# Kernel tuning notes

Measured on AMD Instinct MI355X. Metric: run time of the kernel, lower is better.

The kernel has to match this reference:

```python
import jax, jax.numpy as jnp
import numpy as np

OUT_F, IN_F, GROUP = 4096, 4096, 64  # meta['shape'] = (OUT_F, IN_F), group_size=64, axis=1
TOKENS = 8192  # batch*seq flattened


def dequant(W_q, scale, zero):
    # unpack_4bit_u8: high nibble = first half of rows, low nibble = second half
    hi = (W_q >> 4).astype(jnp.float32)
    lo = (W_q & 0xF).astype(jnp.float32)
    W_r = jnp.concatenate([hi, lo], axis=0)      # [G, GROUP]
    W_r = (W_r - zero) * scale                   # group-wise dequant (axis=1 grouping)
    return W_r.reshape(OUT_F, IN_F)


def setup_inputs() -> dict:
    key = jax.random.key(0)
    k0, k1, k2, k3, k4 = jax.random.split(key, 5)
    G = OUT_F * IN_F // GROUP  # 262144 groups
    x = jax.random.normal(k0, (TOKENS, IN_F), dtype=jnp.float32)
    W_q = jax.random.randint(k1, (G // 2, GROUP), 0, 256, dtype=jnp.int32)  # packed bytes
    scale = jax.random.uniform(k2, (G, 1), dtype=jnp.float32) * 0.01 + 1e-4  # 1/scale from quantizer
    zero = jax.random.uniform(k3, (G, 1), dtype=jnp.float32) * 15.0
    bias = jax.random.normal(k4, (OUT_F,), dtype=jnp.float32)
    return {"x": x, "W_q": W_q, "scale": scale, "zero": zero, "bias": bias}


def reference(x, W_q, scale, zero, bias):
    # HQQMatmulNoCacheDeq.forward: out = x @ dequantize().T + bias
    W_r = dequant(W_q, scale, zero)              # [OUT_F, IN_F]
    return x @ W_r.T + bias                      # [TOKENS, OUT_F]
```

## Files before the change

kernel.cpp:

```cpp
#include <hip/hip_runtime.h>
#include <stdint.h>


typedef __attribute__((ext_vector_type(8))) _Float16 half8;
typedef __attribute__((ext_vector_type(4))) float f32x4;

#define M_DIM 8192
#define N_DIM 4096
#define K_DIM 4096

__device__ __forceinline__ void async16(const void* g, void* l) {
  __builtin_amdgcn_global_load_lds(
      (const __attribute__((address_space(1))) void*)g,
      (__attribute__((address_space(3))) void*)l,
      16, 0, 0);
}

__global__ __launch_bounds__(256) void prep(
    const float* __restrict__ x, const int* __restrict__ Wq,
    const float* __restrict__ scale, const float* __restrict__ zero,
    _Float16* __restrict__ xh, _Float16* __restrict__ wh) {
  const int b = blockIdx.x;
  if (b < 16384) {
    const size_t i = ((size_t)b * 256 + threadIdx.x) * 8;
    f32x4 a = *(const f32x4*)(x + i);
    f32x4 c = *(const f32x4*)(x + i + 4);
    half8 h;
    h[0] = (_Float16)a[0]; h[1] = (_Float16)a[1];
    h[2] = (_Float16)a[2]; h[3] = (_Float16)a[3];
    h[4] = (_Float16)c[0]; h[5] = (_Float16)c[1];
    h[6] = (_Float16)c[2]; h[7] = (_Float16)c[3];
    *(half8*)(xh + i) = h;
  } else {
    const int idx = (b - 16384) * 256 + threadIdx.x;
    const int o  = idx >> 9;
    const int kb = (idx & 511) << 3;
    const int g  = (o << 6) + (kb >> 6);
    const int j  = kb & 63;
    const bool hi = (o < 2048);
    const int* src = Wq + (size_t)(hi ? g : g - 131072) * 64 + j;
    const int4 v0 = *(const int4*)src;
    const int4 v1 = *(const int4*)(src + 4);
    const float s  = scale[g];
    const float nz = -zero[g] * s;
    int raw[8] = {v0.x, v0.y, v0.z, v0.w, v1.x, v1.y, v1.z, v1.w};
    half8 h;
#pragma unroll
    for (int r = 0; r < 8; ++r) {
      const int nib = hi ? ((raw[r] >> 4) & 0xF) : (raw[r] & 0xF);
      h[r] = (_Float16)((float)nib * s + nz);
    }
    *(half8*)(wh + (size_t)o * K_DIM + kb) = h;
  }
}

__global__ __launch_bounds__(512, 2) void gemm_f16_fine(
    const _Float16* __restrict__ A, const _Float16* __restrict__ B,
    const float* __restrict__ bias, float* __restrict__ C) {
  __shared__ _Float16 As[3 * 8192];
  __shared__ _Float16 Bs[3 * 8192];

  const int tid  = threadIdx.x;
  const int wave = tid >> 6;
  const int lane = tid & 63;
  const int quad = lane >> 4;
  const int l16  = lane & 15;
  const int wm   = wave >> 2;
  const int wn   = wave & 3;

  const int bid = blockIdx.x;
  const int swb = (bid & 7) * 64 + (bid >> 3);
  const int m0 = (swb >> 4) * 256;
  const int n0 = (swb & 15) * 256;

  const int srow = tid >> 2;
  const int sg   = (((tid & 3) ^ ((tid >> 3) & 3)) << 3);
  const _Float16* gA0 = A + (size_t)(m0 + srow) * K_DIM + sg;
  const _Float16* gA1 = gA0 + (size_t)128 * K_DIM;
  const _Float16* gB0 = B + (size_t)(n0 + srow) * K_DIM + sg;
  const _Float16* gB1 = gB0 + (size_t)128 * K_DIM;
  const int wst = wave * 512;

  const int fro  = ((quad ^ ((l16 >> 1) & 3)) << 3);
  const int arow = wm * 128 + l16;
  const int brow = wn * 64 + l16;

  f32x4 acc[8][4] = {};

  const int NT = K_DIM / 32;

  async16(gA0,      As + wst);
  async16(gA1,      As + 4096 + wst);
  async16(gB0,      Bs + wst);
  async16(gB1,      Bs + 4096 + wst);
  async16(gA0 + 32, As + 8192 + wst);
  async16(gA1 + 32, As + 8192 + 4096 + wst);
  async16(gB0 + 32, Bs + 8192 + wst);
  async16(gB1 + 32, Bs + 8192 + 4096 + wst);
  asm volatile("s_waitcnt vmcnt(4)" ::: "memory");
  __builtin_amdgcn_s_barrier();

#define KSTEP(SR, SW, T)                                                     \
  {                                                                          \
    half8 aF[4], bF[4];                                                      \
          \
    aF[0] = *(const half8*)(As + (SR) + (arow + 0 * 16) * 32 + fro);         \
    bF[0] = *(const half8*)(Bs + (SR) + (brow + 0 * 16) * 32 + fro);         \
    bF[1] = *(const half8*)(Bs + (SR) + (brow + 1 * 16) * 32 + fro);         \
    bF[2] = *(const half8*)(Bs + (SR) + (brow + 2 * 16) * 32 + fro);         \
    bF[3] = *(const half8*)(Bs + (SR) + (brow + 3 * 16) * 32 + fro);         \
    aF[1] = *(const half8*)(As + (SR) + (arow + 1 * 16) * 32 + fro);         \
    aF[2] = *(const half8*)(As + (SR) + (arow + 2 * 16) * 32 + fro);         \
    aF[3] = *(const half8*)(As + (SR) + (arow + 3 * 16) * 32 + fro);         \
    if ((T) + 2 < NT) {                                                      \
      const int kk = ((T) + 2) * 32;                                         \
      async16(gA0 + kk, As + (SW) + wst);                                    \
      async16(gA1 + kk, As + (SW) + 4096 + wst);                             \
    }                                                                        \
    __builtin_amdgcn_s_barrier();                                            \
    __builtin_amdgcn_s_setprio(1);                                           \
    _Pragma("unroll") for (int i = 0; i < 4; ++i)                            \
      _Pragma("unroll") for (int j = 0; j < 4; ++j)                          \
        acc[i][j] = __builtin_amdgcn_mfma_f32_16x16x32_f16(                  \
            aF[i], bF[j], acc[i][j], 0, 0, 0);                               \
    __builtin_amdgcn_s_setprio(0);                                           \
    __builtin_amdgcn_s_barrier();                                            \
          \
    aF[0] = *(const half8*)(As + (SR) + (arow + 64 + 0 * 16) * 32 + fro);    \
    aF[1] = *(const half8*)(As + (SR) + (arow + 64 + 1 * 16) * 32 + fro);    \
    aF[2] = *(const half8*)(As + (SR) + (arow + 64 + 2 * 16) * 32 + fro);    \
    aF[3] = *(const half8*)(As + (SR) + (arow + 64 + 3 * 16) * 32 + fro);    \
    if ((T) + 2 < NT) {                                                      \
      const int kk = ((T) + 2) * 32;                                         \
      async16(gB0 + kk, Bs + (SW) + wst);                                    \
      async16(gB1 + kk, Bs + (SW) + 4096 + wst);                             \
      asm volatile("s_waitcnt vmcnt(4)" ::: "memory");                       \
    } else {                                                                 \
      asm volatile("s_waitcnt vmcnt(0)" ::: "memory");                       \
    }                                                                        \
    __builtin_amdgcn_s_barrier();                                            \
    __builtin_amdgcn_s_setprio(1);                                           \
    _Pragma("unroll") for (int i = 0; i < 4; ++i)                            \
      _Pragma("unroll") for (int j = 0; j < 4; ++j)                          \
        acc[i + 4][j] = __builtin_amdgcn_mfma_f32_16x16x32_f16(              \
            aF[i], bF[j], acc[i + 4][j], 0, 0, 0);                           \
    __builtin_amdgcn_s_setprio(0);                                           \
    __builtin_amdgcn_s_barrier();                                            \
  }

  for (int T = 0; T < 126; T += 3) {
    KSTEP(0,     16384, T)
    KSTEP(8192,  0,     T + 1)
    KSTEP(16384, 8192,  T + 2)
  }
  KSTEP(0,    16384, 126)
  KSTEP(8192, 0,     127)
#undef KSTEP

#pragma unroll
  for (int j = 0; j < 4; ++j) {
    const int n = n0 + wn * 64 + j * 16 + l16;
    const float bv = bias[n];
#pragma unroll
    for (int i = 0; i < 8; ++i) {
      const int m = m0 + wm * 128 + i * 16 + quad * 4;
      float* p = C + (size_t)m * N_DIM + n;
      f32x4 v = acc[i][j];
      p[0 * N_DIM] = v[0] + bv;
      p[1 * N_DIM] = v[1] + bv;
      p[2 * N_DIM] = v[2] + bv;
      p[3 * N_DIM] = v[3] + bv;
    }
  }
}

__global__ __launch_bounds__(256) void gemm_fp32_fallback(
    const float* __restrict__ x, const int* __restrict__ Wq,
    const float* __restrict__ scale, const float* __restrict__ zero,
    const float* __restrict__ bias, float* __restrict__ C) {
  __shared__ float As[64][16];
  __shared__ float Bs[64][16];
  const int tid = threadIdx.x;
  const int m0 = blockIdx.y * 64;
  const int n0 = blockIdx.x * 64;
  const int tx = tid & 15;
  const int ty = tid >> 4;
  const int lr = tid >> 2;
  const int lc = (tid & 3) << 2;

  float acc[4][4] = {};

  for (int k0 = 0; k0 < K_DIM; k0 += 16) {
    __syncthreads();
    *(f32x4*)&As[lr][lc] = *(const f32x4*)(x + (size_t)(m0 + lr) * K_DIM + k0 + lc);
    {
      const int o = n0 + lr;
      const int k = k0 + lc;
      const int g = (o << 6) + (k >> 6);
      const bool hi = (o < 2048);
      const int* src = Wq + (size_t)(hi ? g : g - 131072) * 64 + (k & 63);
      const int4 v = *(const int4*)src;
      const float s = scale[g];
      const float nz = -zero[g] * s;
      f32x4 b;
      if (hi) {
        b[0] = (float)((v.x >> 4) & 0xF) * s + nz;
        b[1] = (float)((v.y >> 4) & 0xF) * s + nz;
        b[2] = (float)((v.z >> 4) & 0xF) * s + nz;
        b[3] = (float)((v.w >> 4) & 0xF) * s + nz;
      } else {
        b[0] = (float)(v.x & 0xF) * s + nz;
        b[1] = (float)(v.y & 0xF) * s + nz;
        b[2] = (float)(v.z & 0xF) * s + nz;
        b[3] = (float)(v.w & 0xF) * s + nz;
      }
      *(f32x4*)&Bs[lr][lc] = b;
    }
    __syncthreads();
#pragma unroll
    for (int kk = 0; kk < 16; ++kk) {
      float a[4], b[4];
#pragma unroll
      for (int r = 0; r < 4; ++r) a[r] = As[ty * 4 + r][kk];
#pragma unroll
      for (int c = 0; c < 4; ++c) b[c] = Bs[tx * 4 + c][kk];
#pragma unroll
      for (int r = 0; r < 4; ++r)
#pragma unroll
        for (int c = 0; c < 4; ++c) acc[r][c] += a[r] * b[c];
    }
  }
#pragma unroll
  for (int r = 0; r < 4; ++r)
#pragma unroll
    for (int c = 0; c < 4; ++c) {
      const int n = n0 + tx * 4 + c;
      C[(size_t)(m0 + ty * 4 + r) * N_DIM + n] = acc[r][c] + bias[n];
    }
}

extern "C" void kernel_launch(void* const* d_in, const int* in_sizes, int n_in,
                              void* d_out, int out_size, void* d_ws, size_t ws_size,
                              hipStream_t stream) {
  const float* x     = (const float*)d_in[0];
  const int*   Wq    = (const int*)d_in[1];
  const float* scale = (const float*)d_in[2];
  const float* zero  = (const float*)d_in[3];
  const float* bias  = (const float*)d_in[4];
  float* out = (float*)d_out;

  const size_t xh_bytes = (size_t)M_DIM * K_DIM * 2;
  const size_t wh_bytes = (size_t)N_DIM * K_DIM * 2;

  if (ws_size >= xh_bytes + wh_bytes) {
    _Float16* xh = (_Float16*)d_ws;
    _Float16* wh = (_Float16*)((char*)d_ws + xh_bytes);
    prep<<<16384 + 8192, 256, 0, stream>>>(x, Wq, scale, zero, xh, wh);
    gemm_f16_fine<<<(M_DIM / 256) * (N_DIM / 256), 512, 0, stream>>>(xh, wh, bias, out);
  } else {
    dim3 grid(N_DIM / 64, M_DIM / 64);
    gemm_fp32_fallback<<<grid, 64 == 64 ? 256 : 256, 0, stream>>>(x, Wq, scale, zero, bias, out);
  }
}
```

Baseline: 520.0 us.

## Deepen GEMM LDS pipeline to four stages and prefetch next A fragments

The GEMM's shared-memory ring grows from three to four K-stages, so global-to-LDS async loads run three tiles ahead. The two mid-step barriers are removed, leaving one wait and barrier per K-step. The first half of the A fragments for the next step is now read into registers while the current step's second MFMA batch runs. The cost is more LDS per block (128KB), more live fragment registers, and a more delicate wait-count and buffer-reuse scheme.

Result: no change. 512.2 us (-1.5%).

```diff
diff --git a/kernel.cpp b/kernel.cpp
--- a/kernel.cpp
+++ b/kernel.cpp
@@ -54,11 +54,11 @@
   }
 }
 
-__global__ __launch_bounds__(512, 2) void gemm_f16_fine(
+__global__ __launch_bounds__(512, 2) void gemm_f16_pipe(
     const _Float16* __restrict__ A, const _Float16* __restrict__ B,
     const float* __restrict__ bias, float* __restrict__ C) {
-  __shared__ _Float16 As[3 * 8192];
-  __shared__ _Float16 Bs[3 * 8192];
+  __shared__ _Float16 As[4 * 8192];
+  __shared__ _Float16 Bs[4 * 8192];
 
   const int tid  = threadIdx.x;
   const int wave = tid >> 6;
@@ -86,8 +86,7 @@
   const int brow = wn * 64 + l16;
 
   f32x4 acc[8][4] = {};
-
-  const int NT = K_DIM / 32;
+  half8 aFA[4], aFB[4], bF[4];
 
   async16(gA0,      As + wst);
   async16(gA1,      As + 4096 + wst);
@@ -97,64 +96,67 @@
   async16(gA1 + 32, As + 8192 + 4096 + wst);
   async16(gB0 + 32, Bs + 8192 + wst);
   async16(gB1 + 32, Bs + 8192 + 4096 + wst);
+  async16(gA0 + 64, As + 16384 + wst);
+  async16(gA1 + 64, As + 16384 + 4096 + wst);
+  async16(gB0 + 64, Bs + 16384 + wst);
+  async16(gB1 + 64, Bs + 16384 + 4096 + wst);
   asm volatile("s_waitcnt vmcnt(4)" ::: "memory");
   __builtin_amdgcn_s_barrier();
-
-#define KSTEP(SR, SW, T)                                                     \
+  aFA[0] = *(const half8*)(As + (arow + 0 * 16) * 32 + fro);
+  aFA[1] = *(const half8*)(As + (arow + 1 * 16) * 32 + fro);
+  aFA[2] = *(const half8*)(As + (arow + 2 * 16) * 32 + fro);
+  aFA[3] = *(const half8*)(As + (arow + 3 * 16) * 32 + fro);
+
+#define KSTEP(SR, SN, SW, KK2, STAGE_OK, NEXT_OK, VMW)                       \
   {                                                                          \
-    half8 aF[4], bF[4];                                                      \
-          \
-    aF[0] = *(const half8*)(As + (SR) + (arow + 0 * 16) * 32 + fro);         \
     bF[0] = *(const half8*)(Bs + (SR) + (brow + 0 * 16) * 32 + fro);         \
     bF[1] = *(const half8*)(Bs + (SR) + (brow + 1 * 16) * 32 + fro);         \
     bF[2] = *(const half8*)(Bs + (SR) + (brow + 2 * 16) * 32 + fro);         \
     bF[3] = *(const half8*)(Bs + (SR) + (brow + 3 * 16) * 32 + fro);         \
-    aF[1] = *(const half8*)(As + (SR) + (arow + 1 * 16) * 32 + fro);         \
-    aF[2] = *(const half8*)(As + (SR) + (arow + 2 * 16) * 32 + fro);         \
-    aF[3] = *(const half8*)(As + (SR) + (arow + 3 * 16) * 32 + fro);         \
-    if ((T) + 2 < NT) {                                                      \
-      const int kk = ((T) + 2) * 32;                                         \
-      async16(gA0 + kk, As + (SW) + wst);                                    \
-      async16(gA1 + kk, As + (SW) + 4096 + wst);                             \
+    aFB[0] = *(const half8*)(As + (SR) + (arow + 64 + 0 * 16) * 32 + fro);   \
+    aFB[1] = *(const half8*)(As + (SR) + (arow + 64 + 1 * 16) * 32 + fro);   \
+    aFB[2] = *(const half8*)(As + (SR) + (arow + 64 + 2 * 16) * 32 + fro);   \
+    aFB[3] = *(const half8*)(As + (SR) + (arow + 64 + 3 * 16) * 32 + fro);   \
+    if (STAGE_OK) {                                                          \
+      async16(gA0 + (KK2), As + (SW) + wst);                                 \
+      async16(gA1 + (KK2), As + (SW) + 4096 + wst);                          \
     }                                                                        \
-    __builtin_amdgcn_s_barrier();                                            \
     __builtin_amdgcn_s_setprio(1);                                           \
     _Pragma("unroll") for (int i = 0; i < 4; ++i)                            \
       _Pragma("unroll") for (int j = 0; j < 4; ++j)                          \
         acc[i][j] = __builtin_amdgcn_mfma_f32_16x16x32_f16(                  \
-            aF[i], bF[j], acc[i][j], 0, 0, 0);                               \
+            aFA[i], bF[j], acc[i][j], 0, 0, 0);                              \
     __builtin_amdgcn_s_setprio(0);                                           \
-    __builtin_amdgcn_s_barrier();                                            \
-          \
-    aF[0] = *(const half8*)(As + (SR) + (arow + 64 + 0 * 16) * 32 + fro);    \
-    aF[1] = *(const half8*)(As + (SR) + (arow + 64 + 1 * 16) * 32 + fro);    \
-    aF[2] = *(const half8*)(As + (SR) + (arow + 64 + 2 * 16) * 32 + fro);    \
-    aF[3] = *(const half8*)(As + (SR) + (arow + 64 + 3 * 16) * 32 + fro);    \
-    if ((T) + 2 < NT) {                                                      \
-      const int kk = ((T) + 2) * 32;                                         \
-      async16(gB0 + kk, Bs + (SW) + wst);                                    \
-      async16(gB1 + kk, Bs + (SW) + 4096 + wst);                             \
-      asm volatile("s_waitcnt vmcnt(4)" ::: "memory");                       \
-    } else {                                                                 \
-      asm volatile("s_waitcnt vmcnt(0)" ::: "memory");                       \
+    if (NEXT_OK) {                                                           \
+      aFA[0] = *(const half8*)(As + (SN) + (arow + 0 * 16) * 32 + fro);      \
+      aFA[1] = *(const half8*)(As + (SN) + (arow + 1 * 16) * 32 + fro);      \
+      aFA[2] = *(const half8*)(As + (SN) + (arow + 2 * 16) * 32 + fro);      \
+      aFA[3] = *(const half8*)(As + (SN) + (arow + 3 * 16) * 32 + fro);      \
     }                                                                        \
-    __builtin_amdgcn_s_barrier();                                            \
+    if (STAGE_OK) {                                                          \
+      async16(gB0 + (KK2), Bs + (SW) + wst);                                 \
+      async16(gB1 + (KK2), Bs + (SW) + 4096 + wst);                          \
+    }                                                                        \
     __builtin_amdgcn_s_setprio(1);                                           \
     _Pragma("unroll") for (int i = 0; i < 4; ++i)                            \
       _Pragma("unroll") for (int j = 0; j < 4; ++j)                          \
         acc[i + 4][j] = __builtin_amdgcn_mfma_f32_16x16x32_f16(              \
-            aF[i], bF[j], acc[i + 4][j], 0, 0, 0);                           \
+            aFB[i], bF[j], acc[i + 4][j], 0, 0, 0);                          \
     __builtin_amdgcn_s_setprio(0);                                           \
+    asm volatile("s_waitcnt vmcnt(" #VMW ")" ::: "memory");                  \
     __builtin_amdgcn_s_barrier();                                            \
   }
 
-  for (int T = 0; T < 126; T += 3) {
-    KSTEP(0,     16384, T)
-    KSTEP(8192,  0,     T + 1)
-    KSTEP(16384, 8192,  T + 2)
-  }
-  KSTEP(0,    16384, 126)
-  KSTEP(8192, 0,     127)
+  for (int T = 0; T < 124; T += 4) {
+    KSTEP(0,     8192,  24576, (T + 3) * 32, 1, 1, 4)
+    KSTEP(8192,  16384, 0,     (T + 4) * 32, 1, 1, 4)
+    KSTEP(16384, 24576, 8192,  (T + 5) * 32, 1, 1, 4)
+    KSTEP(24576, 0,     16384, (T + 6) * 32, 1, 1, 4)
+  }
+  KSTEP(0,     8192,  24576, 127 * 32, 1, 1, 4)
+  KSTEP(8192,  16384, 0,     0,        0, 1, 0)
+  KSTEP(16384, 24576, 8192,  0,        0, 1, 0)
+  KSTEP(24576, 0,     16384, 0,        0, 0, 0)
 #undef KSTEP
 
 #pragma unroll
@@ -256,9 +258,9 @@
     _Float16* xh = (_Float16*)d_ws;
     _Float16* wh = (_Float16*)((char*)d_ws + xh_bytes);
     prep<<<16384 + 8192, 256, 0, stream>>>(x, Wq, scale, zero, xh, wh);
-    gemm_f16_fine<<<(M_DIM / 256) * (N_DIM / 256), 512, 0, stream>>>(xh, wh, bias, out);
+    gemm_f16_pipe<<<(M_DIM / 256) * (N_DIM / 256), 512, 0, stream>>>(xh, wh, bias, out);
   } else {
     dim3 grid(N_DIM / 64, M_DIM / 64);
-    gemm_fp32_fallback<<<grid, 64 == 64 ? 256 : 256, 0, stream>>>(x, Wq, scale, zero, bias, out);
-  }
-}
+    gemm_fp32_fallback<<<grid, 256, 0, stream>>>(x, Wq, scale, zero, bias, out);
+  }
+}
```
